# Performance work log

Hardware: AMD Instinct MI355X
Metric: run time of the kernel (lower is better)

## Reference

```python
import jax, jax.numpy as jnp
import numpy as np

B, L, C = 64, 2688, 256
W, S, H = 42, 21, 8   # window_size, shift_size, num_heads
HD = C // H
NW = L // W
MLP_H = 4 * C


def _layer_norm(v, g, b, eps=1e-5):
    m = v.mean(-1, keepdims=True)
    var = ((v - m) ** 2).mean(-1, keepdims=True)
    return (v - m) / jnp.sqrt(var + eps) * g + b


def setup_inputs() -> dict:
    key = jax.random.key(0)
    ks = jax.random.split(key, 8)
    std = 0.02
    return {
        "x": jax.random.normal(ks[0], (B, L, C), jnp.float32),
        "norm1_g": jnp.ones((C,), jnp.float32),
        "norm1_b": jnp.zeros((C,), jnp.float32),
        "qkv_w": jax.random.normal(ks[1], (C, 3 * C), jnp.float32) * std,
        "qkv_b": jnp.zeros((3 * C,), jnp.float32),
        "bias_table": jax.random.normal(ks[2], (2 * W - 1, H), jnp.float32) * std,
        "proj_w": jax.random.normal(ks[3], (C, C), jnp.float32) * std,
        "proj_b": jnp.zeros((C,), jnp.float32),
        "norm2_g": jnp.ones((C,), jnp.float32),
        "norm2_b": jnp.zeros((C,), jnp.float32),
        "fc1_w": jax.random.normal(ks[4], (C, MLP_H), jnp.float32) * std,
        "fc1_b": jnp.zeros((MLP_H,), jnp.float32),
        "fc2_w": jax.random.normal(ks[5], (MLP_H, C), jnp.float32) * std,
        "fc2_b": jnp.zeros((C,), jnp.float32),
    }


# ---- static (data-independent) index/mask tables ----
_rel_idx = np.arange(W)[None, :] - np.arange(W)[:, None] + W - 1  # (W, W)
_seg = np.zeros((L,), np.float32)
_seg[-W:-S] = 1.0
_seg[-S:] = 2.0
_mw = _seg.reshape(NW, W)
_am = _mw[:, None, :] - _mw[:, :, None]            # (nW, W, W)
_ATTN_MASK = np.where(_am != 0, -100.0, 0.0).astype(np.float32)


def reference(x, norm1_g, norm1_b, qkv_w, qkv_b, bias_table, proj_w, proj_b,
              norm2_g, norm2_b, fc1_w, fc1_b, fc2_w, fc2_b):
    mask = jnp.asarray(_ATTN_MASK)                  # (nW, W, W)
    scale = HD ** -0.5

    shortcut = x
    h = _layer_norm(x, norm1_g, norm1_b)
    h = jnp.roll(h, -S, axis=1)                     # cyclic shift
    xw = h.reshape(B * NW, W, C)                    # window partition

    qkv = (xw @ qkv_w + qkv_b).reshape(B * NW, W, 3, H, HD).transpose(2, 0, 3, 1, 4)
    q, k, v = qkv[0] * scale, qkv[1], qkv[2]        # each (B_, H, W, HD)
    attn = jnp.einsum('bhnd,bhmd->bhnm', q, k)      # (B_, H, W, W)

    rpb = bias_table[jnp.asarray(_rel_idx)]         # (W, W, H)
    attn = attn + rpb.transpose(2, 0, 1)[None]
    attn = attn.reshape(B, NW, H, W, W) + mask[None, :, None]
    attn = jax.nn.softmax(attn.reshape(B * NW, H, W, W), axis=-1)

    o = jnp.einsum('bhnm,bhmd->bhnd', attn, v)      # (B_, H, W, HD)
    o = o.transpose(0, 2, 1, 3).reshape(B * NW, W, C)
    o = o @ proj_w + proj_b

    h = jnp.roll(o.reshape(B, L, C), S, axis=1)     # reverse shift
    x1 = shortcut + h

    m = _layer_norm(x1, norm2_g, norm2_b)
    m = jax.nn.gelu(m @ fc1_w + fc1_b, approximate=False)
    m = m @ fc2_w + fc2_b
    return x1 + m
```

## Files before the change

### kernel.cpp

```cpp
#include <hip/hip_runtime.h>
#include <hip/hip_bf16.h>

typedef short short8 __attribute__((ext_vector_type(8)));
typedef float floatx4 __attribute__((ext_vector_type(4)));

constexpr int Bc = 64, Lc = 2688, Cc = 256, Wc = 42, Sc = 21;
constexpr int Mrows = Bc * Lc;
constexpr float QSCALE = 0.17677669529663689f;

#define GLOAD_LDS(g, l) __builtin_amdgcn_global_load_lds( \
    (const __attribute__((address_space(1))) void*)(g),   \
    (__attribute__((address_space(3))) void*)(l), 16, 0, 0)
#define BAR() __builtin_amdgcn_s_barrier()
#define WAITV4() asm volatile("s_waitcnt vmcnt(4)" ::: "memory")
#define WAITV0() asm volatile("s_waitcnt vmcnt(0)" ::: "memory")
#define LGKM0() do { asm volatile("s_waitcnt lgkmcnt(0)" ::: "memory"); \
                     __builtin_amdgcn_sched_barrier(0); } while (0)

__global__ __launch_bounds__(256) void transpose_cast_k(const float* __restrict__ w,
                                                        __hip_bfloat16* __restrict__ o,
                                                        int K, int N) {
  __shared__ float tile[32][33];
  int tx = threadIdx.x & 31, ty = threadIdx.x >> 5;
  int n0 = blockIdx.x * 32, k0 = blockIdx.y * 32;
#pragma unroll
  for (int r = 0; r < 32; r += 8)
    tile[ty + r][tx] = w[(size_t)(k0 + ty + r) * N + n0 + tx];
  __syncthreads();
#pragma unroll
  for (int r = 0; r < 32; r += 8)
    o[(size_t)(n0 + ty + r) * K + k0 + tx] = __float2bfloat16(tile[tx][ty + r]);
}

__global__ __launch_bounds__(256) void ln_k(const float* __restrict__ x, const float* __restrict__ g,
                                            const float* __restrict__ bta, __hip_bfloat16* __restrict__ out,
                                            int roll) {
  int row = blockIdx.x * 4 + (threadIdx.x >> 6);
  int lane = threadIdx.x & 63;
  int bb = row / Lc, rl = row - bb * Lc;
  int sl = rl + roll; if (sl >= Lc) sl -= Lc;
  const float4 v = *(const float4*)(x + ((size_t)bb * Lc + sl) * Cc + lane * 4);
  float s = v.x + v.y + v.z + v.w;
#pragma unroll
  for (int o = 1; o < 64; o <<= 1) s += __shfl_xor(s, o, 64);
  float mean = s * (1.0f / Cc);
  float d0 = v.x - mean, d1 = v.y - mean, d2 = v.z - mean, d3 = v.w - mean;
  float s2 = d0 * d0 + d1 * d1 + d2 * d2 + d3 * d3;
#pragma unroll
  for (int o = 1; o < 64; o <<= 1) s2 += __shfl_xor(s2, o, 64);
  float r = rsqrtf(s2 * (1.0f / Cc) + 1e-5f);
  const float4 gg = *(const float4*)(g + lane * 4);
  const float4 bb4 = *(const float4*)(bta + lane * 4);
  __hip_bfloat16 tmp[4];
  tmp[0] = __float2bfloat16(d0 * r * gg.x + bb4.x);
  tmp[1] = __float2bfloat16(d1 * r * gg.y + bb4.y);
  tmp[2] = __float2bfloat16(d2 * r * gg.z + bb4.z);
  tmp[3] = __float2bfloat16(d3 * r * gg.w + bb4.w);
  *(uint2*)(out + (size_t)row * Cc + lane * 4) = *(uint2*)tmp;
}

template <int EPI, int N, int K>
__global__ __launch_bounds__(512, 2) void gemm8(const __hip_bfloat16* __restrict__ A,
                                                const __hip_bfloat16* __restrict__ BT,
                                                const float* __restrict__ bias,
                                                const float* __restrict__ aux,
                                                void* __restrict__ outv) {
  constexpr int NT = K / 64;
  constexpr int NBX = N / 256;
  constexpr int NWG = NBX * (Mrows / 256);
  static_assert(NWG % 8 == 0, "xcd swizzle");
  __shared__ __align__(16) __hip_bfloat16 As[32768];
  __shared__ __align__(16) __hip_bfloat16 Bs[32768];

  const int t = threadIdx.x;
  const int wave = t >> 6, lane = t & 63, q = lane >> 4, lr = lane & 15;
  const int wm = (wave >> 2) * 128, wn = (wave & 3) * 64;

  const int orig = blockIdx.x;
  const int wgid = (orig & 7) * (NWG / 8) + (orig >> 3);
  const int bx = wgid % NBX, by = wgid / NBX;
  const int n0 = bx * 256, m0 = by * 256;

  auto srcoff = [&](int c) {
    int o = c * 16;
    int u = o ^ (((o >> 8) & 3) << 4);
    return (size_t)(u >> 6) * K + (size_t)((u >> 4) & 3) * 8;
  };
  const __hip_bfloat16* sA0 = A + (size_t)m0 * K + srcoff(t);
  const __hip_bfloat16* sA1 = A + (size_t)m0 * K + srcoff(512 + t);
  const __hip_bfloat16* sB0 = BT + (size_t)n0 * K + srcoff(t);
  const __hip_bfloat16* sB1 = BT + (size_t)n0 * K + srcoff(512 + t);

  int offA[8], offB[4];
#pragma unroll
  for (int i = 0; i < 8; i++) {
    int lin = (wm + i * 16 + lr) * 64 + q * 16;
    offA[i] = lin ^ (((lin >> 8) & 3) << 4);
  }
#pragma unroll
  for (int j = 0; j < 4; j++) {
    int lin = (wn + j * 16 + lr) * 64 + q * 16;
    offB[j] = lin ^ (((lin >> 8) & 3) << 4);
  }

  floatx4 acc[8][4] = {};
  short8 afr[4], bfr[4];

#define STAGE(s0, s1, region, koff) do {            \
    __hip_bfloat16* l_ = (region) + wave * 512;     \
    GLOAD_LDS((s0) + (koff), l_);                   \
    GLOAD_LDS((s1) + (koff), l_ + 4096); } while (0)

#define LDA4(base_, mq_) { \
    const char* Ab_ = (const char*)(base_); \
    _Pragma("unroll") for (int i_ = 0; i_ < 4; i_++) afr[i_] = *(const short8*)(Ab_ + offA[(mq_) * 4 + i_]); }
#define LDB4(base_) { \
    const char* Bb_ = (const char*)(base_); \
    _Pragma("unroll") for (int j_ = 0; j_ < 4; j_++) bfr[j_] = *(const short8*)(Bb_ + offB[j_]); }
#define MFMA16(mq_) \
    __builtin_amdgcn_s_setprio(1); \
    _Pragma("unroll") for (int i_ = 0; i_ < 4; i_++) \
    _Pragma("unroll") for (int j_ = 0; j_ < 4; j_++) \
      acc[(mq_) * 4 + i_][j_] = __builtin_amdgcn_mfma_f32_16x16x32_bf16(afr[i_], bfr[j_], acc[(mq_) * 4 + i_][j_], 0, 0, 0); \
    __builtin_amdgcn_s_setprio(0);

  STAGE(sA0, sA1, As + 0 * 8192, 0);
  STAGE(sB0, sB1, Bs + 0 * 8192, 0);
  STAGE(sA0, sA1, As + 1 * 8192, 32);
  STAGE(sB0, sB1, Bs + 1 * 8192, 32);
  WAITV0();
  BAR();

  for (int kt = 0; kt < NT - 1; ++kt) {
    const int buf = kt & 1, nbuf = buf ^ 1;
    const int kn = (kt + 1) * 64;
    __hip_bfloat16* A0 = As + (buf * 2 + 0) * 8192;
    __hip_bfloat16* A1 = As + (buf * 2 + 1) * 8192;
    __hip_bfloat16* B0 = Bs + (buf * 2 + 0) * 8192;
    __hip_bfloat16* B1 = Bs + (buf * 2 + 1) * 8192;
    LDA4(A0, 0); LDB4(B0);
    STAGE(sA0, sA1, As + (nbuf * 2 + 0) * 8192, kn);
    BAR(); LGKM0(); MFMA16(0); BAR();
    LDA4(A0, 1);
    STAGE(sB0, sB1, Bs + (nbuf * 2 + 0) * 8192, kn);
    BAR(); LGKM0(); MFMA16(1);
    WAITV4(); BAR();
    LDA4(A1, 0); LDB4(B1);
    STAGE(sA0, sA1, As + (nbuf * 2 + 1) * 8192, kn + 32);
    BAR(); LGKM0(); MFMA16(0); BAR();
    LDA4(A1, 1);
    STAGE(sB0, sB1, Bs + (nbuf * 2 + 1) * 8192, kn + 32);
    BAR(); LGKM0(); MFMA16(1);
    WAITV4(); BAR();
  }
  {
    const int buf = (NT - 1) & 1;
    __hip_bfloat16* A0 = As + (buf * 2 + 0) * 8192;
    __hip_bfloat16* A1 = As + (buf * 2 + 1) * 8192;
    __hip_bfloat16* B0 = Bs + (buf * 2 + 0) * 8192;
    __hip_bfloat16* B1 = Bs + (buf * 2 + 1) * 8192;
    LDA4(A0, 0); LDB4(B0);
    BAR(); LGKM0(); MFMA16(0); BAR();
    LDA4(A0, 1);
    BAR(); LGKM0(); MFMA16(1);
    WAITV0(); BAR();
    LDA4(A1, 0); LDB4(B1);
    BAR(); LGKM0(); MFMA16(0); BAR();
    LDA4(A1, 1);
    LGKM0(); MFMA16(1);
  }

  if (EPI == 0) {
    BAR();
    char* Tc = (char*)((wave < 4) ? (As + wave * 8192) : (Bs + (wave - 4) * 8192));
#pragma unroll
    for (int mf = 0; mf < 8; mf++) {
#pragma unroll
      for (int rg = 0; rg < 4; rg++) {
        int row = mf * 16 + q * 4 + rg;
        int sw = ((row >> 2) & 3) << 5;
#pragma unroll
        for (int nf = 0; nf < 4; nf++) {
          int lcol = nf * 16 + lr;
          int gcol = n0 + wn + lcol;
          float v = acc[mf][nf][rg] + bias[gcol];
          if (gcol < 256) v *= QSCALE;
          *(__hip_bfloat16*)(Tc + row * 128 + ((lcol * 2) ^ sw)) = __float2bfloat16(v);
        }
      }
    }
    LGKM0();
#pragma unroll
    for (int it = 0; it < 16; it++) {
      int id = it * 64 + lane;
      int row = id >> 3, cg = id & 7;
      short8 val = *(const short8*)(Tc + row * 128 + ((cg * 16) ^ (((row >> 2) & 3) << 5)));
      *(short8*)((__hip_bfloat16*)outv + (size_t)(m0 + wm + row) * N + (n0 + wn + cg * 8)) = val;
    }
  } else {
#pragma unroll
    for (int mf = 0; mf < 8; mf++) {
#pragma unroll
      for (int rg = 0; rg < 4; rg++) {
        int row = m0 + wm + mf * 16 + q * 4 + rg;
        int bb = row / Lc;
        int rl = row - bb * Lc;
        int l = rl + Sc; if (l >= Lc) l -= Lc;
#pragma unroll
        for (int nf = 0; nf < 4; nf++) {
          int col = n0 + wn + nf * 16 + lr;
          float v = acc[mf][nf][rg] + bias[col];
          size_t o = ((size_t)bb * Lc + l) * Cc + col;
          ((float*)outv)[o] = aux[o] + v;
        }
      }
    }
  }
#undef STAGE
#undef LDA4
#undef LDB4
#undef MFMA16
}

__global__ __launch_bounds__(512, 2) void mlp_k(const float* __restrict__ x1,
                                                const __hip_bfloat16* __restrict__ fc1T,
                                                const float* __restrict__ b1,
                                                const __hip_bfloat16* __restrict__ fc2T,
                                                const float* __restrict__ b2,
                                                const float* __restrict__ n2g,
                                                const float* __restrict__ n2b,
                                                float* __restrict__ out) {
  __shared__ __align__(16) __hip_bfloat16 mA[128 * 256];
  __shared__ __align__(16) __hip_bfloat16 act[128 * 256];
  const int t = threadIdx.x, wave = t >> 6, lane = t & 63, q = lane >> 4, lr = lane & 15;
  const int wm = (wave >> 2) * 64, wn = (wave & 3) * 64;
  const int m0 = blockIdx.x * 128;

  {
    const float4 gg = *(const float4*)(n2g + lane * 4);
    const float4 bv = *(const float4*)(n2b + lane * 4);
#pragma unroll
    for (int i = 0; i < 16; i++) {
      int row = wave * 16 + i;
      const float4 v = *(const float4*)(x1 + (size_t)(m0 + row) * 256 + lane * 4);
      float s = v.x + v.y + v.z + v.w;
#pragma unroll
      for (int o = 1; o < 64; o <<= 1) s += __shfl_xor(s, o, 64);
      float mean = s * (1.0f / 256.0f);
      float d0 = v.x - mean, d1 = v.y - mean, d2 = v.z - mean, d3 = v.w - mean;
      float s2 = d0 * d0 + d1 * d1 + d2 * d2 + d3 * d3;
#pragma unroll
      for (int o = 1; o < 64; o <<= 1) s2 += __shfl_xor(s2, o, 64);
      float r = rsqrtf(s2 * (1.0f / 256.0f) + 1e-5f);
      __hip_bfloat16 tmp[4];
      tmp[0] = __float2bfloat16(d0 * r * gg.x + bv.x);
      tmp[1] = __float2bfloat16(d1 * r * gg.y + bv.y);
      tmp[2] = __float2bfloat16(d2 * r * gg.z + bv.z);
      tmp[3] = __float2bfloat16(d3 * r * gg.w + bv.w);
      *(uint2*)((char*)mA + row * 512 + ((lane * 8) ^ ((row & 7) << 4))) = *(uint2*)tmp;
    }
  }

  floatx4 acc2[4][4];
#pragma unroll
  for (int mf = 0; mf < 4; mf++)
#pragma unroll
    for (int rg = 0; rg < 4; rg++) {
      int row = m0 + wm + mf * 16 + q * 4 + rg;
#pragma unroll
      for (int nf = 0; nf < 4; nf++)
        acc2[mf][nf][rg] = x1[(size_t)row * 256 + wn + nf * 16 + lr];
    }
  __syncthreads();

  for (int c = 0; c < 4; c++) {
    floatx4 acc1[4][4] = {};
    const __hip_bfloat16* B1p = fc1T + (size_t)(c * 256) * 256;
#pragma unroll
    for (int ks = 0; ks < 8; ks++) {
      short8 af[4], bf[4];
#pragma unroll
      for (int i = 0; i < 4; i++) {
        int row = wm + i * 16 + lr;
        af[i] = *(const short8*)((char*)mA + row * 512 + ((ks * 64 + q * 16) ^ ((row & 7) << 4)));
      }
#pragma unroll
      for (int j = 0; j < 4; j++)
        bf[j] = *(const short8*)(B1p + (size_t)(wn + j * 16 + lr) * 256 + ks * 32 + q * 8);
#pragma unroll
      for (int i = 0; i < 4; i++)
#pragma unroll
        for (int j = 0; j < 4; j++)
          acc1[i][j] = __builtin_amdgcn_mfma_f32_16x16x32_bf16(af[i], bf[j], acc1[i][j], 0, 0, 0);
    }
    __syncthreads();
#pragma unroll
    for (int mf = 0; mf < 4; mf++)
#pragma unroll
      for (int rg = 0; rg < 4; rg++) {
        int row = wm + mf * 16 + q * 4 + rg;
#pragma unroll
        for (int nf = 0; nf < 4; nf++) {
          int col = wn + nf * 16 + lr;
          float v = acc1[mf][nf][rg] + b1[c * 256 + col];
          float u = v * (0.7978845608028654f + 0.03567740813630012f * v * v);
          v = v * __builtin_amdgcn_rcpf(1.0f + __expf(-2.0f * u));
          *(__hip_bfloat16*)((char*)act + row * 512 + ((col * 2) ^ ((row & 7) << 4))) = __float2bfloat16(v);
        }
      }
    __syncthreads();
#pragma unroll
    for (int ks = 0; ks < 8; ks++) {
      short8 af[4], bf[4];
#pragma unroll
      for (int i = 0; i < 4; i++) {
        int row = wm + i * 16 + lr;
        af[i] = *(const short8*)((char*)act + row * 512 + ((ks * 64 + q * 16) ^ ((row & 7) << 4)));
      }
#pragma unroll
      for (int j = 0; j < 4; j++)
        bf[j] = *(const short8*)(fc2T + (size_t)(wn + j * 16 + lr) * 1024 + c * 256 + ks * 32 + q * 8);
#pragma unroll
      for (int i = 0; i < 4; i++)
#pragma unroll
        for (int j = 0; j < 4; j++)
          acc2[i][j] = __builtin_amdgcn_mfma_f32_16x16x32_bf16(af[i], bf[j], acc2[i][j], 0, 0, 0);
    }
  }

#pragma unroll
  for (int mf = 0; mf < 4; mf++)
#pragma unroll
    for (int rg = 0; rg < 4; rg++) {
      int row = m0 + wm + mf * 16 + q * 4 + rg;
#pragma unroll
      for (int nf = 0; nf < 4; nf++) {
        int col = wn + nf * 16 + lr;
        out[(size_t)row * 256 + col] = acc2[mf][nf][rg] + b2[col];
      }
    }
}

constexpr int PSTR = 72;
constexpr int PSZ = 48 * PSTR;
constexpr int VTSZ = 32 * PSTR;

__global__ __launch_bounds__(256) void attn_k(const __hip_bfloat16* __restrict__ qkv,
                                              const float* __restrict__ bias_table,
                                              __hip_bfloat16* __restrict__ o_buf) {
  __shared__ __align__(16) __hip_bfloat16 smem[4 * PSZ + 4 * VTSZ];
  __shared__ float btab[83 * 8];
  const int t = threadIdx.x, wave = t >> 6, lane = t & 63, q = lane >> 4, lr = lane & 15;
  const int win = blockIdx.x >> 1;
  const int h = (blockIdx.x & 1) * 4 + wave;

  for (int i = t; i < (4 * PSZ + 4 * VTSZ) / 8; i += 256) ((uint4*)smem)[i] = uint4{0, 0, 0, 0};
  for (int i = t; i < 83 * 8; i += 256) btab[i] = bias_table[i];
  __syncthreads();

  __hip_bfloat16* Pw = smem + wave * PSZ;
  __hip_bfloat16* VTw = smem + 4 * PSZ + wave * VTSZ;
  const __hip_bfloat16* qbase = qkv + (size_t)win * 42 * 768 + h * 32;
  const __hip_bfloat16* kbase = qbase + 256;
  const __hip_bfloat16* vbase = qbase + 512;

  for (int c = lane; c < 42 * 4; c += 64) {
    int j = c >> 2, d0 = (c & 3) * 8;
    short8 vv = *(const short8*)(vbase + (size_t)j * 768 + d0);
#pragma unroll
    for (int e = 0; e < 8; e++) ((short*)VTw)[(d0 + e) * PSTR + j] = vv[e];
  }

  short8 qf[3], kf[3];
#pragma unroll
  for (int mt = 0; mt < 3; mt++) {
    int i = mt * 16 + lr; if (i > 41) i = 41;
    qf[mt] = *(const short8*)(qbase + (size_t)i * 768 + q * 8);
  }
#pragma unroll
  for (int nt = 0; nt < 3; nt++) {
    int j = nt * 16 + lr; if (j > 41) j = 41;
    kf[nt] = *(const short8*)(kbase + (size_t)j * 768 + q * 8);
  }
  floatx4 sacc[3][3] = {};
#pragma unroll
  for (int mt = 0; mt < 3; mt++)
#pragma unroll
    for (int nt = 0; nt < 3; nt++)
      sacc[mt][nt] = __builtin_amdgcn_mfma_f32_16x16x32_bf16(qf[mt], kf[nt], sacc[mt][nt], 0, 0, 0);

  const bool lastwin = ((win & 63) == 63);
#pragma unroll
  for (int mt = 0; mt < 3; mt++) {
#pragma unroll
    for (int rg = 0; rg < 4; rg++) {
      int row = mt * 16 + q * 4 + rg;
      float sv[3];
      float mx = -1e30f;
#pragma unroll
      for (int nt = 0; nt < 3; nt++) {
        int col = nt * 16 + lr;
        float s = sacc[mt][nt][rg];
        int ri = col - row + 41; ri = ri < 0 ? 0 : (ri > 82 ? 82 : ri);
        s += btab[ri * 8 + h];
        if (lastwin && ((row < 21) != (col < 21))) s -= 100.0f;
        if (col >= 42) s = -1e30f;
        sv[nt] = s;
        mx = fmaxf(mx, s);
      }
#pragma unroll
      for (int o = 1; o < 16; o <<= 1) mx = fmaxf(mx, __shfl_xor(mx, o, 64));
      float sum = 0.0f;
#pragma unroll
      for (int nt = 0; nt < 3; nt++) { float e = __expf(sv[nt] - mx); sv[nt] = e; sum += e; }
#pragma unroll
      for (int o = 1; o < 16; o <<= 1) sum += __shfl_xor(sum, o, 64);
      float inv = 1.0f / sum;
#pragma unroll
      for (int nt = 0; nt < 3; nt++) Pw[row * PSTR + nt * 16 + lr] = __float2bfloat16(sv[nt] * inv);
    }
  }
  __syncthreads();

  floatx4 oacc[3][2] = {};
#pragma unroll
  for (int ks = 0; ks < 2; ks++) {
    short8 pf[3], vf[2];
#pragma unroll
    for (int mt = 0; mt < 3; mt++) pf[mt] = *(const short8*)(Pw + (mt * 16 + lr) * PSTR + ks * 32 + q * 8);
#pragma unroll
    for (int nt = 0; nt < 2; nt++) vf[nt] = *(const short8*)(VTw + (nt * 16 + lr) * PSTR + ks * 32 + q * 8);
#pragma unroll
    for (int mt = 0; mt < 3; mt++)
#pragma unroll
      for (int nt = 0; nt < 2; nt++)
        oacc[mt][nt] = __builtin_amdgcn_mfma_f32_16x16x32_bf16(pf[mt], vf[nt], oacc[mt][nt], 0, 0, 0);
  }
#pragma unroll
  for (int mt = 0; mt < 3; mt++) {
#pragma unroll
    for (int rg = 0; rg < 4; rg++) {
      int row = mt * 16 + q * 4 + rg;
      if (row < 42) {
#pragma unroll
        for (int nt = 0; nt < 2; nt++) {
          int col = nt * 16 + lr;
          o_buf[((size_t)win * 42 + row) * 256 + h * 32 + col] = __float2bfloat16(oacc[mt][nt][rg]);
        }
      }
    }
  }
}

extern "C" void kernel_launch(void* const* d_in, const int* in_sizes, int n_in,
                              void* d_out, int out_size, void* d_ws, size_t ws_size,
                              hipStream_t stream) {
  const float* x       = (const float*)d_in[0];
  const float* norm1_g = (const float*)d_in[1];
  const float* norm1_b = (const float*)d_in[2];
  const float* qkv_w   = (const float*)d_in[3];
  const float* qkv_b   = (const float*)d_in[4];
  const float* btab    = (const float*)d_in[5];
  const float* proj_w  = (const float*)d_in[6];
  const float* proj_b  = (const float*)d_in[7];
  const float* norm2_g = (const float*)d_in[8];
  const float* norm2_b = (const float*)d_in[9];
  const float* fc1_w   = (const float*)d_in[10];
  const float* fc1_b   = (const float*)d_in[11];
  const float* fc2_w   = (const float*)d_in[12];
  const float* fc2_b   = (const float*)d_in[13];
  float* out = (float*)d_out;

  char* ws = (char*)d_ws;
  size_t off = 0;
  auto alloc = [&](size_t bytes) { char* p = ws + off; off += (bytes + 255) & ~(size_t)255; return p; };
  __hip_bfloat16* wT_qkv  = (__hip_bfloat16*)alloc((size_t)768 * 256 * 2);
  __hip_bfloat16* wT_proj = (__hip_bfloat16*)alloc((size_t)256 * 256 * 2);
  __hip_bfloat16* wT_fc1  = (__hip_bfloat16*)alloc((size_t)1024 * 256 * 2);
  __hip_bfloat16* wT_fc2  = (__hip_bfloat16*)alloc((size_t)256 * 1024 * 2);
  __hip_bfloat16* buf88   = (__hip_bfloat16*)alloc((size_t)Mrows * 256 * 2);
  __hip_bfloat16* buf352  = (__hip_bfloat16*)alloc((size_t)Mrows * 1024 * 2);

  transpose_cast_k<<<dim3(768 / 32, 256 / 32), 256, 0, stream>>>(qkv_w, wT_qkv, 256, 768);
  transpose_cast_k<<<dim3(256 / 32, 256 / 32), 256, 0, stream>>>(proj_w, wT_proj, 256, 256);
  transpose_cast_k<<<dim3(1024 / 32, 256 / 32), 256, 0, stream>>>(fc1_w, wT_fc1, 256, 1024);
  transpose_cast_k<<<dim3(256 / 32, 1024 / 32), 256, 0, stream>>>(fc2_w, wT_fc2, 1024, 256);

  ln_k<<<Mrows / 4, 256, 0, stream>>>(x, norm1_g, norm1_b, buf88, Sc);

  gemm8<0, 768, 256><<<dim3(3 * (Mrows / 256)), 512, 0, stream>>>(buf88, wT_qkv, qkv_b, nullptr, buf352);

  attn_k<<<(Mrows / Wc) * 2, 256, 0, stream>>>(buf352, btab, buf88);

  gemm8<1, 256, 256><<<dim3(Mrows / 256), 512, 0, stream>>>(buf88, wT_proj, proj_b, x, out);

  mlp_k<<<Mrows / 128, 512, 0, stream>>>(out, wT_fc1, fc1_b, wT_fc2, fc2_b, norm2_g, norm2_b, out);

  (void)in_sizes; (void)n_in; (void)out_size; (void)ws_size;
}
```

Measured before the change: 1.209 ms.

## Restructure fused MLP into 64-wide hidden chunks to raise occupancy

The fused LN2+fc1+GELU+fc2 kernel now walks the 1024-wide hidden dimension in 16 chunks of 64 instead of 4 chunks of 256. This shrinks the activation LDS buffer to 128x64 and the per-wave fc1 accumulators. fc2 is remapped so each wave owns a 32x128 output tile. The residual load moves from the prologue to the epilogue, which lowers register pressure, and launch bounds are raised to target 4 blocks per CU. In exchange the kernel hits more barriers per row tile and issues smaller MFMA batches per chunk, with fc2 B-operand loads spread over more iterations.

```diff
diff --git a/kernel.cpp b/kernel.cpp
--- a/kernel.cpp
+++ b/kernel.cpp
@@ -222,7 +222,7 @@
 #undef MFMA16
 }
 
-__global__ __launch_bounds__(512, 2) void mlp_k(const float* __restrict__ x1,
+__global__ __launch_bounds__(512, 4) void mlp_k(const float* __restrict__ x1,
                                                 const __hip_bfloat16* __restrict__ fc1T,
                                                 const float* __restrict__ b1,
                                                 const __hip_bfloat16* __restrict__ fc2T,
@@ -231,10 +231,11 @@
                                                 const float* __restrict__ n2b,
                                                 float* __restrict__ out) {
   __shared__ __align__(16) __hip_bfloat16 mA[128 * 256];
-  __shared__ __align__(16) __hip_bfloat16 act[128 * 256];
+  __shared__ __align__(16) __hip_bfloat16 act[128 * 64];
   const int t = threadIdx.x, wave = t >> 6, lane = t & 63, q = lane >> 4, lr = lane & 15;
-  const int wm = (wave >> 2) * 64, wn = (wave & 3) * 64;
   const int m0 = blockIdx.x * 128;
+  const int r1 = (wave >> 1) * 32, c1 = (wave & 1) * 32;
+  const int r2 = (wave >> 1) * 32, c2 = (wave & 1) * 128;
 
   {
     const float4 gg = *(const float4*)(n2g + lane * 4);
@@ -260,83 +261,73 @@
       *(uint2*)((char*)mA + row * 512 + ((lane * 8) ^ ((row & 7) << 4))) = *(uint2*)tmp;
     }
   }
-
-  floatx4 acc2[4][4];
-#pragma unroll
-  for (int mf = 0; mf < 4; mf++)
-#pragma unroll
-    for (int rg = 0; rg < 4; rg++) {
-      int row = m0 + wm + mf * 16 + q * 4 + rg;
-#pragma unroll
-      for (int nf = 0; nf < 4; nf++)
-        acc2[mf][nf][rg] = x1[(size_t)row * 256 + wn + nf * 16 + lr];
-    }
   __syncthreads();
 
-  for (int c = 0; c < 4; c++) {
-    floatx4 acc1[4][4] = {};
-    const __hip_bfloat16* B1p = fc1T + (size_t)(c * 256) * 256;
+  floatx4 acc2[2][8] = {};
+
+  for (int cc = 0; cc < 16; cc++) {
+    floatx4 acc1[2][2] = {};
 #pragma unroll
     for (int ks = 0; ks < 8; ks++) {
-      short8 af[4], bf[4];
-#pragma unroll
-      for (int i = 0; i < 4; i++) {
-        int row = wm + i * 16 + lr;
+      short8 af[2], bf[2];
+#pragma unroll
+      for (int i = 0; i < 2; i++) {
+        int row = r1 + i * 16 + lr;
         af[i] = *(const short8*)((char*)mA + row * 512 + ((ks * 64 + q * 16) ^ ((row & 7) << 4)));
       }
 #pragma unroll
-      for (int j = 0; j < 4; j++)
-        bf[j] = *(const short8*)(B1p + (size_t)(wn + j * 16 + lr) * 256 + ks * 32 + q * 8);
-#pragma unroll
-      for (int i = 0; i < 4; i++)
-#pragma unroll
-        for (int j = 0; j < 4; j++)
+      for (int j = 0; j < 2; j++)
+        bf[j] = *(const short8*)(fc1T + (size_t)(cc * 64 + c1 + j * 16 + lr) * 256 + ks * 32 + q * 8);
+#pragma unroll
+      for (int i = 0; i < 2; i++)
+#pragma unroll
+        for (int j = 0; j < 2; j++)
           acc1[i][j] = __builtin_amdgcn_mfma_f32_16x16x32_bf16(af[i], bf[j], acc1[i][j], 0, 0, 0);
     }
-    __syncthreads();
-#pragma unroll
-    for (int mf = 0; mf < 4; mf++)
+    LGKM0(); BAR();
+#pragma unroll
+    for (int i = 0; i < 2; i++)
 #pragma unroll
       for (int rg = 0; rg < 4; rg++) {
-        int row = wm + mf * 16 + q * 4 + rg;
-#pragma unroll
-        for (int nf = 0; nf < 4; nf++) {
-          int col = wn + nf * 16 + lr;
-          float v = acc1[mf][nf][rg] + b1[c * 256 + col];
+        int row = r1 + i * 16 + q * 4 + rg;
+#pragma unroll
+        for (int j = 0; j < 2; j++) {
+          int colc = c1 + j * 16 + lr;
+          float v = acc1[i][j][rg] + b1[cc * 64 + colc];
           float u = v * (0.7978845608028654f + 0.03567740813630012f * v * v);
           v = v * __builtin_amdgcn_rcpf(1.0f + __expf(-2.0f * u));
-          *(__hip_bfloat16*)((char*)act + row * 512 + ((col * 2) ^ ((row & 7) << 4))) = __float2bfloat16(v);
+          *(__hip_bfloat16*)((char*)act + row * 128 + ((colc * 2) ^ ((row & 7) << 4))) = __float2bfloat16(v);
         }
       }
-    __syncthreads();
-#pragma unroll
-    for (int ks = 0; ks < 8; ks++) {
-      short8 af[4], bf[4];
-#pragma unroll
-      for (int i = 0; i < 4; i++) {
-        int row = wm + i * 16 + lr;
-        af[i] = *(const short8*)((char*)act + row * 512 + ((ks * 64 + q * 16) ^ ((row & 7) << 4)));
-      }
-#pragma unroll
-      for (int j = 0; j < 4; j++)
-        bf[j] = *(const short8*)(fc2T + (size_t)(wn + j * 16 + lr) * 1024 + c * 256 + ks * 32 + q * 8);
-#pragma unroll
-      for (int i = 0; i < 4; i++)
-#pragma unroll
-        for (int j = 0; j < 4; j++)
-          acc2[i][j] = __builtin_amdgcn_mfma_f32_16x16x32_bf16(af[i], bf[j], acc2[i][j], 0, 0, 0);
-    }
-  }
-
-#pragma unroll
-  for (int mf = 0; mf < 4; mf++)
+    LGKM0(); BAR();
+#pragma unroll
+    for (int ks = 0; ks < 2; ks++) {
+      short8 af2[2];
+#pragma unroll
+      for (int i = 0; i < 2; i++) {
+        int row = r2 + i * 16 + lr;
+        af2[i] = *(const short8*)((char*)act + row * 128 + ((ks * 64 + q * 16) ^ ((row & 7) << 4)));
+      }
+#pragma unroll
+      for (int j = 0; j < 8; j++) {
+        short8 bf2 = *(const short8*)(fc2T + (size_t)(c2 + j * 16 + lr) * 1024 + cc * 64 + ks * 32 + q * 8);
+#pragma unroll
+        for (int i = 0; i < 2; i++)
+          acc2[i][j] = __builtin_amdgcn_mfma_f32_16x16x32_bf16(af2[i], bf2, acc2[i][j], 0, 0, 0);
+      }
+    }
+  }
+
+#pragma unroll
+  for (int i = 0; i < 2; i++)
 #pragma unroll
     for (int rg = 0; rg < 4; rg++) {
-      int row = m0 + wm + mf * 16 + q * 4 + rg;
-#pragma unroll
-      for (int nf = 0; nf < 4; nf++) {
-        int col = wn + nf * 16 + lr;
-        out[(size_t)row * 256 + col] = acc2[mf][nf][rg] + b2[col];
+      int row = m0 + r2 + i * 16 + q * 4 + rg;
+#pragma unroll
+      for (int j = 0; j < 8; j++) {
+        int col = c2 + j * 16 + lr;
+        size_t o = (size_t)row * 256 + col;
+        out[o] = x1[o] + acc2[i][j][rg] + b2[col];
       }
     }
 }
```

After: 1.477 ms. 22.2% more time.
